# Optimization experiments

Hardware: AMD Instinct MI355X
Metric: run time of the kernel (lower is better)

The kernel has to match this reference:

```python
import jax, jax.numpy as jnp
import numpy as np

N_BR, D, SD, RH, MH, UD, NOBS, B = 4, 256, 64, 64, 128, 16, 25, 32768
LN_EPS = 1e-5

def setup_inputs() -> dict:
    key = jax.random.key(0)
    ks = jax.random.split(key, 16)
    meas_in = D + SD
    rnn_in = RH + UD
    return {
        "z_dyn": jax.random.normal(ks[0], (B, D), jnp.float32),
        "z_static": jax.random.normal(ks[1], (B, SD), jnp.float32),
        "dt": jnp.ones((1,), jnp.float32),
        "ut": jax.random.normal(ks[2], (B, UD), jnp.float32),
        "gates": jax.random.normal(ks[3], (N_BR, D), jnp.float32) * 0.1,
        "W1": jax.random.normal(ks[4], (N_BR, MH, meas_in), jnp.float32) * (1.0 / np.sqrt(meas_in)),
        "b1": jnp.zeros((N_BR, MH), jnp.float32),
        "gamma": jnp.ones((N_BR, MH), jnp.float32),
        "beta": jnp.zeros((N_BR, MH), jnp.float32),
        "W2": jax.random.normal(ks[5], (N_BR, RH, MH), jnp.float32) * (1.0 / np.sqrt(MH)),
        "b2": jnp.zeros((N_BR, RH), jnp.float32),
        "lam_real": jnp.zeros((N_BR, RH), jnp.float32),
        "lam_imag": jax.random.normal(ks[6], (N_BR, RH), jnp.float32) * 0.1,
        "Bmat": jax.random.normal(ks[7], (N_BR, RH, rnn_in), jnp.float32) * (1.0 / np.sqrt(rnn_in)),
        "Wout": jax.random.normal(ks[8], (N_BR, D, RH), jnp.float32) * (1.0 / np.sqrt(RH)),
        "C": jax.random.normal(ks[9], (NOBS, D), jnp.float32) * (1.0 / np.sqrt(D)),
        "D": jax.random.normal(ks[10], (NOBS, UD), jnp.float32) * (1.0 / np.sqrt(UD)),
    }

def reference(z_dyn, z_static, dt, ut, gates, W1, b1, gamma, beta, W2, b2,
              lam_real, lam_imag, Bmat, Wout, C, D):
    ut_dt = ut * dt  # [B,u]
    n, Bsz = gates.shape[0], z_dyn.shape[0]
    # spectral gate per branch: [n,B,d]
    zg = z_dyn[None] * jax.nn.sigmoid(gates)[:, None, :]
    zs = jnp.broadcast_to(z_static[None], (n, Bsz, z_static.shape[-1]))
    x = jnp.concatenate([zg, zs], axis=-1)  # [n,B,meas_in]
    # measurement MLP: Linear -> LayerNorm -> GELU -> Linear
    h = jnp.einsum('nbi,nhi->nbh', x, W1) + b1[:, None, :]
    mu = h.mean(-1, keepdims=True)
    var = ((h - mu) ** 2).mean(-1, keepdims=True)
    h = (h - mu) / jnp.sqrt(var + LN_EPS) * gamma[:, None, :] + beta[:, None, :]
    h = jax.nn.gelu(h, approximate=False)
    g = jnp.einsum('nbh,noh->nbo', h, W2) + b2[:, None, :]  # [n,B,rnn_h]
    u_b = jnp.broadcast_to(ut_dt[None], (n, Bsz, ut_dt.shape[-1]))
    inp = jnp.concatenate([g, u_b], axis=-1)  # [n,B,rnn_h+u]
    b_inp = jnp.einsum('nbi,nhi->nbh', inp, Bmat)
    # complex recurrence step from h0 = 0 (as in forward())
    mag = jax.nn.sigmoid(lam_real) * 0.99
    lam_r = mag * jnp.cos(lam_imag)
    lam_i = mag * jnp.sin(lam_imag)
    h0r = jnp.zeros_like(b_inp)
    h0i = jnp.zeros_like(b_inp)
    h_real = h0r * lam_r[:, None, :] - h0i * lam_i[:, None, :] + b_inp
    # output projection per branch, summed over branches
    z_next = jnp.einsum('nbh,ndh->bd', h_real, Wout)
    yt = z_next @ C.T + ut_dt @ D.T
    return (z_next, yt)
```

## Files before the change

### kernel.cpp

```cpp
#include <hip/hip_runtime.h>
#include <hip/hip_bf16.h>

#define B_ROWS 32768
#define LN_EPS 1e-5f

typedef __bf16 bf16;
using bf16x8 = __attribute__((ext_vector_type(8))) __bf16;
using f32x4  = __attribute__((ext_vector_type(4))) float;


__device__ __forceinline__ float gelu_exact(float x) {
  float s = x * 0.70710678118f;
  float a = fabsf(s);
  float t = __builtin_amdgcn_rcpf(fmaf(0.3275911f, a, 1.0f));
  float p = fmaf(fmaf(fmaf(fmaf(1.061405429f, t, -1.453152027f),
                           t, 1.421413741f), t, -0.284496736f), t, 0.254829592f) * t;
  float e = __expf(-s * s);
  float er = fmaf(-p, e, 1.0f);
  er = copysignf(er, s);
  return 0.5f * x * (1.0f + er);
}

__global__ __launch_bounds__(256) void prep_weights1(
    const float* __restrict__ gates, const float* __restrict__ W1,
    const float* __restrict__ Bmat,  const float* __restrict__ W2,
    const float* __restrict__ b2,    const float* __restrict__ Wout,
    const float* __restrict__ Cm,
    bf16* __restrict__ W1sw, float* __restrict__ Mtmp, float* __restrict__ cvec,
    float* __restrict__ CW)
{
  const int stride = gridDim.x * blockDim.x;
  const int id = blockIdx.x * blockDim.x + threadIdx.x;
  for (int o = id; o < 512 * 320; o += stride) {
    int e = o & 7, m = (o >> 3) & 15, q2 = (o >> 7) & 3, rest = o >> 9;
    int kk = rest % 10, G = rest / 10;
    int n = G * 16 + m, k = kk * 32 + q2 * 8 + e;
    float wv = W1[n * 320 + k];
    if (k < 256) {
      float g = gates[(n >> 7) * 256 + k];
      wv *= 1.f / (1.f + __expf(-g));
    }
    W1sw[o] = (bf16)wv;
  }
  for (int i = id; i < 4 * 64 * 128; i += stride) {
    int n = i >> 13, r = (i >> 7) & 63, h = i & 127;
    float s = 0.f;
    for (int j = 0; j < 64; ++j)
      s += Bmat[(n * 64 + r) * 80 + j] * W2[(n * 64 + j) * 128 + h];
    Mtmp[i] = s;
  }
  for (int i = id; i < 256; i += stride) {
    int n = i >> 6, r = i & 63;
    float s = 0.f;
    for (int j = 0; j < 64; ++j)
      s += Bmat[(n * 64 + r) * 80 + j] * b2[n * 64 + j];
    cvec[i] = s;
  }
  for (int i = id; i < 25 * 256; i += stride) {
    int o = i >> 8, nr = i & 255;
    float s = 0.f;
    for (int d = 0; d < 256; ++d)
      s += Cm[o * 256 + d] * Wout[((nr >> 6) * 256 + d) * 64 + (nr & 63)];
    CW[i] = s;
  }
}

__global__ __launch_bounds__(256) void prep_weights2(
    const float* __restrict__ Wout, const float* __restrict__ Bmat,
    const float* __restrict__ Mtmp, const float* __restrict__ cvec,
    const float* __restrict__ CW,   const float* __restrict__ Dm,
    bf16* __restrict__ Psw)
{
  const int stride = gridDim.x * blockDim.x;
  const int id = blockIdx.x * blockDim.x + threadIdx.x;
  for (int o = id; o < 320 * 544; o += stride) {
    int e = o & 7, m = (o >> 3) & 15, q2 = (o >> 7) & 3, rest = o >> 9;
    int kk2 = rest % 17, G2 = rest / 17;
    int dd = G2 * 16 + m, cc = kk2 * 32 + q2 * 8 + e;
    float s = 0.f;
    if (dd < 281) {
      const bool isC = (dd >= 256);
      const int oo = dd - 256;
      if (cc < 512) {
        int n = cc >> 7, h = cc & 127;
        for (int r = 0; r < 64; ++r) {
          float wv = isC ? CW[(oo * 4 + n) * 64 + r] : Wout[(n * 256 + dd) * 64 + r];
          s += wv * Mtmp[(n * 64 + r) * 128 + h];
        }
      } else if (cc < 528) {
        int u = cc - 512;
        for (int n = 0; n < 4; ++n)
          for (int r = 0; r < 64; ++r) {
            float wv = isC ? CW[(oo * 4 + n) * 64 + r] : Wout[(n * 256 + dd) * 64 + r];
            s += wv * Bmat[(n * 64 + r) * 80 + 64 + u];
          }
        if (isC) s += Dm[oo * 16 + u];
      } else if (cc == 528) {
        for (int n = 0; n < 4; ++n)
          for (int r = 0; r < 64; ++r) {
            float wv = isC ? CW[(oo * 4 + n) * 64 + r] : Wout[(n * 256 + dd) * 64 + r];
            s += wv * cvec[n * 64 + r];
          }
      }
    }
    Psw[o] = (bf16)s;
  }
}

__global__ __launch_bounds__(256, 2) void fused_main(
    const float* __restrict__ zdyn, const float* __restrict__ zst,
    const float* __restrict__ ut,   const float* __restrict__ dtp,
    const bf16* __restrict__ W1sw,  const bf16* __restrict__ Psw,
    const float* __restrict__ b1,   const float* __restrict__ gamma,
    const float* __restrict__ beta,
    float* __restrict__ Z, float* __restrict__ yt)
{
  __shared__ __align__(16) bf16 Xs[64 * 320];
  __shared__ __align__(16) bf16 Hc[64 * 128];
  __shared__ __align__(16) bf16 Ht[64 * 32];
  __shared__ float sgam[512], sbet[512], sb1[512];
  __shared__ float red[256], red2[256];
  __shared__ float smu[64], srs[64];

  const int t = threadIdx.x;
  const int lane = t & 63, m16 = lane & 15, q = lane >> 4;
  const int w = t >> 6;
  const int rowBase = blockIdx.x * 64;

  sgam[t] = gamma[t]; sbet[t] = beta[t]; sb1[t] = b1[t];
  sgam[t + 256] = gamma[t + 256]; sbet[t + 256] = beta[t + 256]; sb1[t + 256] = b1[t + 256];

  #pragma unroll
  for (int a = 0; a < 10; ++a) {
    int g = a * 256 + t;
    int row = g / 40, pos = g - row * 40;
    int kk = pos >> 2, pq = pos & 3;
    int lq = pq ^ ((row >> 1) & 3);
    int col = kk * 32 + lq * 8;
    const float* src = (col < 256) ? &zdyn[(size_t)(rowBase + row) * 256 + col]
                                   : &zst[(size_t)(rowBase + row) * 64 + (col - 256)];
    float4 v0 = *(const float4*)src;
    float4 v1 = *(const float4*)(src + 4);
    bf16x8 o;
    o[0]=(bf16)v0.x; o[1]=(bf16)v0.y; o[2]=(bf16)v0.z; o[3]=(bf16)v0.w;
    o[4]=(bf16)v1.x; o[5]=(bf16)v1.y; o[6]=(bf16)v1.z; o[7]=(bf16)v1.w;
    *(bf16x8*)&Xs[(size_t)((kk * 64 + row) * 4 + pq) * 8] = o;
  }
  {
    const float dtv = dtp[0];
    int r = t >> 2, pq = t & 3;
    int lq = pq ^ ((r >> 1) & 3);
    bf16x8 o;
    #pragma unroll
    for (int e = 0; e < 8; ++e) {
      int ci = lq * 8 + e;
      float v = (ci < 16) ? ut[(size_t)(rowBase + r) * 16 + ci] * dtv
                          : (ci == 16 ? 1.f : 0.f);
      o[e] = (bf16)v;
    }
    *(bf16x8*)&Ht[t * 8] = o;
  }
  __syncthreads();

  f32x4 accZ[4][5];
  #pragma unroll
  for (int i = 0; i < 4; ++i)
    #pragma unroll
    for (int j = 0; j < 5; ++j)
      #pragma unroll
      for (int r = 0; r < 4; ++r) accZ[i][j][r] = 0.f;

  #pragma unroll 1
  for (int c = 0; c < 4; ++c) {
    f32x4 acc1[4][2];
    #pragma unroll
    for (int i = 0; i < 4; ++i)
      #pragma unroll
      for (int j = 0; j < 2; ++j)
        #pragma unroll
        for (int r = 0; r < 4; ++r) acc1[i][j][r] = 0.f;

    #pragma unroll
    for (int kk = 0; kk < 10; ++kk) {
      bf16x8 bfr[2];
      #pragma unroll
      for (int j = 0; j < 2; ++j) {
        int G = c * 8 + w * 2 + j;
        bfr[j] = *(const bf16x8*)&W1sw[(size_t)(((G * 10 + kk) * 4 + q) * 16 + m16) * 8];
      }
      bf16x8 af[4];
      #pragma unroll
      for (int i = 0; i < 4; ++i) {
        int row = i * 16 + m16;
        af[i] = *(const bf16x8*)&Xs[(size_t)((kk * 64 + row) * 4 + (q ^ ((row >> 1) & 3))) * 8];
      }
      #pragma unroll
      for (int i = 0; i < 4; ++i)
        #pragma unroll
        for (int j = 0; j < 2; ++j)
          acc1[i][j] = __builtin_amdgcn_mfma_f32_16x16x32_bf16(af[i], bfr[j], acc1[i][j], 0, 0, 0);
    }

    __syncthreads();
    #pragma unroll
    for (int j = 0; j < 2; ++j) {
      int tc = w * 32 + j * 16 + m16;
      float bb = sb1[c * 128 + tc];
      int tk = tc >> 5, ci = tc & 31;
      int lq2 = ci >> 3, e2 = ci & 7;
      #pragma unroll
      for (int i = 0; i < 4; ++i)
        #pragma unroll
        for (int rr = 0; rr < 4; ++rr) {
          int row = i * 16 + q * 4 + rr;
          Hc[((tk * 64 + row) * 4 + (lq2 ^ ((row >> 1) & 3))) * 8 + e2] =
              (bf16)(acc1[i][j][rr] + bb);
        }
    }
    __syncthreads();
    {
      int row = t >> 2, tk = t & 3;
      float s = 0.f, s2 = 0.f;
      #pragma unroll
      for (int ch = 0; ch < 4; ++ch) {
        bf16x8 hv = *(const bf16x8*)&Hc[((tk * 64 + row) * 4 + ch) * 8];
        #pragma unroll
        for (int e = 0; e < 8; ++e) { float v = (float)hv[e]; s += v; s2 = fmaf(v, v, s2); }
      }
      red[t] = s; red2[t] = s2;
    }
    __syncthreads();
    if (t < 64) {
      float ss = red[t * 4] + red[t * 4 + 1] + red[t * 4 + 2] + red[t * 4 + 3];
      float qq = red2[t * 4] + red2[t * 4 + 1] + red2[t * 4 + 2] + red2[t * 4 + 3];
      float mu = ss * 0.0078125f;
      float var = qq * 0.0078125f - mu * mu;
      smu[t] = mu;
      srs[t] = rsqrtf(fmaxf(var, 0.f) + LN_EPS);
    }
    __syncthreads();
    #pragma unroll
    for (int a = 0; a < 4; ++a) {
      int id = a * 256 + t;
      int pq = id & 3, row = (id >> 2) & 63, tk = id >> 8;
      int lq = pq ^ ((row >> 1) & 3);
      int gcol = c * 128 + tk * 32 + lq * 8;
      bf16x8 hv = *(const bf16x8*)&Hc[id * 8];
      float mu = smu[row], rs = srs[row];
      bf16x8 ov;
      #pragma unroll
      for (int e = 0; e < 8; ++e) {
        float v = ((float)hv[e] - mu) * rs;
        v = fmaf(v, sgam[gcol + e], sbet[gcol + e]);
        ov[e] = (bf16)gelu_exact(v);
      }
      *(bf16x8*)&Hc[id * 8] = ov;
    }
    __syncthreads();

    #pragma unroll
    for (int tk = 0; tk < 4; ++tk) {
      int kk2 = c * 4 + tk;
      bf16x8 af[4], bfr[5];
      #pragma unroll
      for (int i = 0; i < 4; ++i) {
        int row = i * 16 + m16;
        af[i] = *(const bf16x8*)&Hc[((tk * 64 + row) * 4 + (q ^ ((row >> 1) & 3))) * 8];
      }
      #pragma unroll
      for (int j = 0; j < 5; ++j) {
        int G2 = w * 5 + j;
        bfr[j] = *(const bf16x8*)&Psw[(size_t)(((G2 * 17 + kk2) * 4 + q) * 16 + m16) * 8];
      }
      #pragma unroll
      for (int i = 0; i < 4; ++i)
        #pragma unroll
        for (int j = 0; j < 5; ++j)
          accZ[i][j] = __builtin_amdgcn_mfma_f32_16x16x32_bf16(af[i], bfr[j], accZ[i][j], 0, 0, 0);
    }
  }

  {
    bf16x8 af[4], bfr[5];
    #pragma unroll
    for (int i = 0; i < 4; ++i) {
      int row = i * 16 + m16;
      af[i] = *(const bf16x8*)&Ht[(row * 4 + (q ^ ((row >> 1) & 3))) * 8];
    }
    #pragma unroll
    for (int j = 0; j < 5; ++j) {
      int G2 = w * 5 + j;
      bfr[j] = *(const bf16x8*)&Psw[(size_t)(((G2 * 17 + 16) * 4 + q) * 16 + m16) * 8];
    }
    #pragma unroll
    for (int i = 0; i < 4; ++i)
      #pragma unroll
      for (int j = 0; j < 5; ++j)
        accZ[i][j] = __builtin_amdgcn_mfma_f32_16x16x32_bf16(af[i], bfr[j], accZ[i][j], 0, 0, 0);
  }

  #pragma unroll
  for (int i = 0; i < 4; ++i)
    #pragma unroll
    for (int j = 0; j < 5; ++j) {
      int col = w * 80 + j * 16 + m16;
      #pragma unroll
      for (int rr = 0; rr < 4; ++rr) {
        int row = rowBase + i * 16 + q * 4 + rr;
        if (col < 256) Z[(size_t)row * 256 + col] = accZ[i][j][rr];
        else if (col < 281) yt[(size_t)row * 25 + (col - 256)] = accZ[i][j][rr];
      }
    }
}

extern "C" void kernel_launch(void* const* d_in, const int* in_sizes, int n_in,
                              void* d_out, int out_size, void* d_ws, size_t ws_size,
                              hipStream_t stream) {
  const float* zdyn  = (const float*)d_in[0];
  const float* zst   = (const float*)d_in[1];
  const float* dtp   = (const float*)d_in[2];
  const float* ut    = (const float*)d_in[3];
  const float* gates = (const float*)d_in[4];
  const float* W1    = (const float*)d_in[5];
  const float* b1    = (const float*)d_in[6];
  const float* gamma = (const float*)d_in[7];
  const float* beta  = (const float*)d_in[8];
  const float* W2    = (const float*)d_in[9];
  const float* b2    = (const float*)d_in[10];
  const float* Bmat  = (const float*)d_in[13];
  const float* Wout  = (const float*)d_in[14];
  const float* Cm    = (const float*)d_in[15];
  const float* Dm    = (const float*)d_in[16];

  char* ws = (char*)d_ws;
  bf16*  W1sw = (bf16*)(ws);
  bf16*  Psw  = (bf16*)(ws + 327680);
  float* Mtmp = (float*)(ws + 675840);
  float* cvec = (float*)(ws + 806912);
  float* CW   = (float*)(ws + 807936);

  float* Z  = (float*)d_out;
  float* yt = Z + (size_t)B_ROWS * 256;

  hipLaunchKernelGGL(prep_weights1, dim3(128), dim3(256), 0, stream,
                     gates, W1, Bmat, W2, b2, Wout, Cm, W1sw, Mtmp, cvec, CW);
  hipLaunchKernelGGL(prep_weights2, dim3(256), dim3(256), 0, stream,
                     Wout, Bmat, Mtmp, cvec, CW, Dm, Psw);
  hipLaunchKernelGGL(fused_main, dim3(512), dim3(256), 0, stream,
                     zdyn, zst, ut, dtp, W1sw, Psw, b1, gamma, beta, Z, yt);
}
```

Before: 183.6 us.

## Compute LayerNorm stats in registers via shuffles and fuse GELU before LDS store

Adds the bias and computes LayerNorm partial sums directly from the MFMA accumulators, using lane shuffles and a small partial-sum array, instead of storing pre-LN values to LDS and reading them back. Normalization, affine and GELU are then applied in registers and written once to a re-laid-out Hc buffer. This removes one LDS round trip and a barrier per chunk. __syncthreads is also replaced with a raw lgkmcnt wait plus s_barrier. The risks are scattered scalar bf16 stores to LDS, which can cause bank conflicts, and more register pressure under the 2-waves launch bound.

After: 190.8 us. 3.9% more time.

```diff
diff --git a/kernel.cpp b/kernel.cpp
--- a/kernel.cpp
+++ b/kernel.cpp
@@ -8,6 +8,10 @@
 using bf16x8 = __attribute__((ext_vector_type(8))) __bf16;
 using f32x4  = __attribute__((ext_vector_type(4))) float;
 
+
+__device__ __forceinline__ void lds_barrier() {
+  asm volatile("s_waitcnt lgkmcnt(0)\n\ts_barrier" ::: "memory");
+}
 
 __device__ __forceinline__ float gelu_exact(float x) {
   float s = x * 0.70710678118f;
@@ -118,17 +122,18 @@
   __shared__ __align__(16) bf16 Xs[64 * 320];
   __shared__ __align__(16) bf16 Hc[64 * 128];
   __shared__ __align__(16) bf16 Ht[64 * 32];
-  __shared__ float sgam[512], sbet[512], sb1[512];
-  __shared__ float red[256], red2[256];
-  __shared__ float smu[64], srs[64];
+  __shared__ float sb1[512], sgam[512], sbet[512];
+  __shared__ float2 spart[64 * 17];
+  __shared__ __align__(16) float smu[64], srs[64];
 
   const int t = threadIdx.x;
   const int lane = t & 63, m16 = lane & 15, q = lane >> 4;
   const int w = t >> 6;
   const int rowBase = blockIdx.x * 64;
 
-  sgam[t] = gamma[t]; sbet[t] = beta[t]; sb1[t] = b1[t];
-  sgam[t + 256] = gamma[t + 256]; sbet[t + 256] = beta[t + 256]; sb1[t + 256] = b1[t + 256];
+  sb1[t] = b1[t];   sb1[t + 256] = b1[t + 256];
+  sgam[t] = gamma[t]; sgam[t + 256] = gamma[t + 256];
+  sbet[t] = beta[t];  sbet[t + 256] = beta[t + 256];
 
   #pragma unroll
   for (int a = 0; a < 10; ++a) {
@@ -160,7 +165,7 @@
     }
     *(bf16x8*)&Ht[t * 8] = o;
   }
-  __syncthreads();
+  lds_barrier();
 
   f32x4 accZ[4][5];
   #pragma unroll
@@ -201,71 +206,76 @@
           acc1[i][j] = __builtin_amdgcn_mfma_f32_16x16x32_bf16(af[i], bfr[j], acc1[i][j], 0, 0, 0);
     }
 
-    __syncthreads();
-    #pragma unroll
-    for (int j = 0; j < 2; ++j) {
-      int tc = w * 32 + j * 16 + m16;
-      float bb = sb1[c * 128 + tc];
-      int tk = tc >> 5, ci = tc & 31;
-      int lq2 = ci >> 3, e2 = ci & 7;
-      #pragma unroll
-      for (int i = 0; i < 4; ++i)
+    {
+      float b0v = sb1[c * 128 + w * 32 + m16];
+      float b1v = sb1[c * 128 + w * 32 + 16 + m16];
+      const int slot = w * 4 + (m16 >> 2);
+      #pragma unroll
+      for (int i = 0; i < 4; ++i) {
+        #pragma unroll
+        for (int rr = 0; rr < 4; ++rr) {
+          float v0 = acc1[i][0][rr] + b0v;
+          float v1 = acc1[i][1][rr] + b1v;
+          acc1[i][0][rr] = v0;
+          acc1[i][1][rr] = v1;
+          float s  = v0 + v1;
+          float s2 = fmaf(v0, v0, v1 * v1);
+          s  += __shfl_xor(s, 1);  s  += __shfl_xor(s, 2);
+          s2 += __shfl_xor(s2, 1); s2 += __shfl_xor(s2, 2);
+          if ((m16 & 3) == 0) {
+            int row = i * 16 + q * 4 + rr;
+            spart[row * 17 + slot] = make_float2(s, s2);
+          }
+        }
+      }
+    }
+    lds_barrier();
+    if (t < 64) {
+      float s = 0.f, s2 = 0.f;
+      #pragma unroll
+      for (int m = 0; m < 16; ++m) {
+        float2 p = spart[t * 17 + m];
+        s += p.x; s2 += p.y;
+      }
+      float mu = s * 0.0078125f;
+      float var = s2 * 0.0078125f - mu * mu;
+      smu[t] = mu;
+      srs[t] = rsqrtf(fmaxf(var, 0.f) + LN_EPS);
+    }
+    lds_barrier();
+
+    {
+      float g0 = sgam[c * 128 + w * 32 + m16];
+      float g1 = sgam[c * 128 + w * 32 + 16 + m16];
+      float be0 = sbet[c * 128 + w * 32 + m16];
+      float be1 = sbet[c * 128 + w * 32 + 16 + m16];
+      int col0 = w * 32 + m16, col1 = w * 32 + 16 + m16;
+      int cq0 = col0 >> 3, cq1 = col1 >> 3;
+      #pragma unroll
+      for (int i = 0; i < 4; ++i) {
+        f32x4 mu4 = *(const f32x4*)&smu[i * 16 + q * 4];
+        f32x4 rs4 = *(const f32x4*)&srs[i * 16 + q * 4];
         #pragma unroll
         for (int rr = 0; rr < 4; ++rr) {
           int row = i * 16 + q * 4 + rr;
-          Hc[((tk * 64 + row) * 4 + (lq2 ^ ((row >> 1) & 3))) * 8 + e2] =
-              (bf16)(acc1[i][j][rr] + bb);
+          int sw = (row >> 1) & 3;
+          float v0 = fmaf((acc1[i][0][rr] - mu4[rr]) * rs4[rr], g0, be0);
+          float v1 = fmaf((acc1[i][1][rr] - mu4[rr]) * rs4[rr], g1, be1);
+          Hc[row * 128 + (cq0 ^ sw) * 8 + (col0 & 7)] = (bf16)gelu_exact(v0);
+          Hc[row * 128 + (cq1 ^ sw) * 8 + (col1 & 7)] = (bf16)gelu_exact(v1);
         }
-    }
-    __syncthreads();
-    {
-      int row = t >> 2, tk = t & 3;
-      float s = 0.f, s2 = 0.f;
-      #pragma unroll
-      for (int ch = 0; ch < 4; ++ch) {
-        bf16x8 hv = *(const bf16x8*)&Hc[((tk * 64 + row) * 4 + ch) * 8];
-        #pragma unroll
-        for (int e = 0; e < 8; ++e) { float v = (float)hv[e]; s += v; s2 = fmaf(v, v, s2); }
-      }
-      red[t] = s; red2[t] = s2;
-    }
-    __syncthreads();
-    if (t < 64) {
-      float ss = red[t * 4] + red[t * 4 + 1] + red[t * 4 + 2] + red[t * 4 + 3];
-      float qq = red2[t * 4] + red2[t * 4 + 1] + red2[t * 4 + 2] + red2[t * 4 + 3];
-      float mu = ss * 0.0078125f;
-      float var = qq * 0.0078125f - mu * mu;
-      smu[t] = mu;
-      srs[t] = rsqrtf(fmaxf(var, 0.f) + LN_EPS);
-    }
-    __syncthreads();
-    #pragma unroll
-    for (int a = 0; a < 4; ++a) {
-      int id = a * 256 + t;
-      int pq = id & 3, row = (id >> 2) & 63, tk = id >> 8;
-      int lq = pq ^ ((row >> 1) & 3);
-      int gcol = c * 128 + tk * 32 + lq * 8;
-      bf16x8 hv = *(const bf16x8*)&Hc[id * 8];
-      float mu = smu[row], rs = srs[row];
-      bf16x8 ov;
-      #pragma unroll
-      for (int e = 0; e < 8; ++e) {
-        float v = ((float)hv[e] - mu) * rs;
-        v = fmaf(v, sgam[gcol + e], sbet[gcol + e]);
-        ov[e] = (bf16)gelu_exact(v);
-      }
-      *(bf16x8*)&Hc[id * 8] = ov;
-    }
-    __syncthreads();
-
-    #pragma unroll
-    for (int tk = 0; tk < 4; ++tk) {
-      int kk2 = c * 4 + tk;
+      }
+    }
+    lds_barrier();
+
+    #pragma unroll
+    for (int t2 = 0; t2 < 4; ++t2) {
+      int kk2 = c * 4 + t2;
       bf16x8 af[4], bfr[5];
       #pragma unroll
       for (int i = 0; i < 4; ++i) {
         int row = i * 16 + m16;
-        af[i] = *(const bf16x8*)&Hc[((tk * 64 + row) * 4 + (q ^ ((row >> 1) & 3))) * 8];
+        af[i] = *(const bf16x8*)&Hc[row * 128 + (((t2 * 4 + q) ^ ((row >> 1) & 3))) * 8];
       }
       #pragma unroll
       for (int j = 0; j < 5; ++j) {
@@ -303,11 +313,11 @@
   for (int i = 0; i < 4; ++i)
     #pragma unroll
     for (int j = 0; j < 5; ++j) {
-      int col = w * 80 + j * 16 + m16;
+      int col = (w * 5 + j) * 16 + m16;
       #pragma unroll
       for (int rr = 0; rr < 4; ++rr) {
         int row = rowBase + i * 16 + q * 4 + rr;
-        if (col < 256) Z[(size_t)row * 256 + col] = accZ[i][j][rr];
+        if (col < 256)      Z[(size_t)row * 256 + col] = accZ[i][j][rr];
         else if (col < 281) yt[(size_t)row * 25 + (col - 256)] = accZ[i][j][rr];
       }
     }
```

## Software-pipeline first GEMM of next chunk with second GEMM, lighter barriers

Applied to the files above, without the earlier changes.

Restructures the chunk loop so the first-layer MFMA for chunk c+1 is interleaved with the second-layer MFMA for chunk c, letting their independent work overlap within each wave. It also drops the separate LayerNorm statistics pass and its two barriers: each thread now recomputes mean and rstd from the partial sums. The remaining __syncthreads are replaced by a raw s_waitcnt lgkmcnt(0) + s_barrier. Keeping two accumulator sets live raises register pressure, which under launch_bounds(256,2) risks spills, and the inline-asm barrier skips waiting on global memory traffic.

Result: slower. 270.0 us (+47.1%).

```diff
diff --git a/kernel.cpp b/kernel.cpp
--- a/kernel.cpp
+++ b/kernel.cpp
@@ -8,6 +8,10 @@
 using bf16x8 = __attribute__((ext_vector_type(8))) __bf16;
 using f32x4  = __attribute__((ext_vector_type(4))) float;
 
+
+__device__ __forceinline__ void lds_barrier() {
+  asm volatile("s_waitcnt lgkmcnt(0)\n\ts_barrier" ::: "memory");
+}
 
 __device__ __forceinline__ float gelu_exact(float x) {
   float s = x * 0.70710678118f;
@@ -118,17 +122,17 @@
   __shared__ __align__(16) bf16 Xs[64 * 320];
   __shared__ __align__(16) bf16 Hc[64 * 128];
   __shared__ __align__(16) bf16 Ht[64 * 32];
-  __shared__ float sgam[512], sbet[512], sb1[512];
+  __shared__ float sb1[512], sgam[512], sbet[512];
   __shared__ float red[256], red2[256];
-  __shared__ float smu[64], srs[64];
 
   const int t = threadIdx.x;
   const int lane = t & 63, m16 = lane & 15, q = lane >> 4;
   const int w = t >> 6;
   const int rowBase = blockIdx.x * 64;
 
-  sgam[t] = gamma[t]; sbet[t] = beta[t]; sb1[t] = b1[t];
-  sgam[t + 256] = gamma[t + 256]; sbet[t + 256] = beta[t + 256]; sb1[t + 256] = b1[t + 256];
+  sb1[t] = b1[t];   sb1[t + 256] = b1[t + 256];
+  sgam[t] = gamma[t]; sgam[t + 256] = gamma[t + 256];
+  sbet[t] = beta[t];  sbet[t + 256] = beta[t + 256];
 
   #pragma unroll
   for (int a = 0; a < 10; ++a) {
@@ -160,7 +164,7 @@
     }
     *(bf16x8*)&Ht[t * 8] = o;
   }
-  __syncthreads();
+  lds_barrier();
 
   f32x4 accZ[4][5];
   #pragma unroll
@@ -170,38 +174,50 @@
       #pragma unroll
       for (int r = 0; r < 4; ++r) accZ[i][j][r] = 0.f;
 
-  #pragma unroll 1
-  for (int c = 0; c < 4; ++c) {
-    f32x4 acc1[4][2];
+  f32x4 acc1[4][2];
+
+  auto p1_step = [&](int cc, int kk) {
+    bf16x8 bfr0 = *(const bf16x8*)&W1sw[(size_t)((((cc * 8 + w * 2 + 0) * 10 + kk) * 4 + q) * 16 + m16) * 8];
+    bf16x8 bfr1 = *(const bf16x8*)&W1sw[(size_t)((((cc * 8 + w * 2 + 1) * 10 + kk) * 4 + q) * 16 + m16) * 8];
+    #pragma unroll
+    for (int i = 0; i < 4; ++i) {
+      int row = i * 16 + m16;
+      bf16x8 af = *(const bf16x8*)&Xs[(size_t)((kk * 64 + row) * 4 + (q ^ ((row >> 1) & 3))) * 8];
+      acc1[i][0] = __builtin_amdgcn_mfma_f32_16x16x32_bf16(af, bfr0, acc1[i][0], 0, 0, 0);
+      acc1[i][1] = __builtin_amdgcn_mfma_f32_16x16x32_bf16(af, bfr1, acc1[i][1], 0, 0, 0);
+    }
+  };
+  auto p2_step = [&](int cc, int t2) {
+    int kk2 = cc * 4 + t2;
+    bf16x8 bfr[5];
+    #pragma unroll
+    for (int j = 0; j < 5; ++j)
+      bfr[j] = *(const bf16x8*)&Psw[(size_t)((((w * 5 + j) * 17 + kk2) * 4 + q) * 16 + m16) * 8];
+    #pragma unroll
+    for (int i = 0; i < 4; ++i) {
+      int row = i * 16 + m16;
+      bf16x8 af = *(const bf16x8*)&Hc[((t2 * 64 + row) * 4 + (q ^ ((row >> 1) & 3))) * 8];
+      #pragma unroll
+      for (int j = 0; j < 5; ++j)
+        accZ[i][j] = __builtin_amdgcn_mfma_f32_16x16x32_bf16(af, bfr[j], accZ[i][j], 0, 0, 0);
+    }
+  };
+  auto p1_zero = [&]() {
     #pragma unroll
     for (int i = 0; i < 4; ++i)
       #pragma unroll
       for (int j = 0; j < 2; ++j)
         #pragma unroll
         for (int r = 0; r < 4; ++r) acc1[i][j][r] = 0.f;
-
-    #pragma unroll
-    for (int kk = 0; kk < 10; ++kk) {
-      bf16x8 bfr[2];
-      #pragma unroll
-      for (int j = 0; j < 2; ++j) {
-        int G = c * 8 + w * 2 + j;
-        bfr[j] = *(const bf16x8*)&W1sw[(size_t)(((G * 10 + kk) * 4 + q) * 16 + m16) * 8];
-      }
-      bf16x8 af[4];
-      #pragma unroll
-      for (int i = 0; i < 4; ++i) {
-        int row = i * 16 + m16;
-        af[i] = *(const bf16x8*)&Xs[(size_t)((kk * 64 + row) * 4 + (q ^ ((row >> 1) & 3))) * 8];
-      }
-      #pragma unroll
-      for (int i = 0; i < 4; ++i)
-        #pragma unroll
-        for (int j = 0; j < 2; ++j)
-          acc1[i][j] = __builtin_amdgcn_mfma_f32_16x16x32_bf16(af[i], bfr[j], acc1[i][j], 0, 0, 0);
-    }
-
-    __syncthreads();
+  };
+
+  p1_zero();
+  #pragma unroll
+  for (int kk = 0; kk < 10; ++kk) p1_step(0, kk);
+
+  #pragma unroll 1
+  for (int c = 0; c < 4; ++c) {
+    lds_barrier();
     #pragma unroll
     for (int j = 0; j < 2; ++j) {
       int tc = w * 32 + j * 16 + m16;
@@ -217,7 +233,7 @@
               (bf16)(acc1[i][j][rr] + bb);
         }
     }
-    __syncthreads();
+    lds_barrier();
     {
       int row = t >> 2, tk = t & 3;
       float s = 0.f, s2 = 0.f;
@@ -229,24 +245,19 @@
       }
       red[t] = s; red2[t] = s2;
     }
-    __syncthreads();
-    if (t < 64) {
-      float ss = red[t * 4] + red[t * 4 + 1] + red[t * 4 + 2] + red[t * 4 + 3];
-      float qq = red2[t * 4] + red2[t * 4 + 1] + red2[t * 4 + 2] + red2[t * 4 + 3];
-      float mu = ss * 0.0078125f;
-      float var = qq * 0.0078125f - mu * mu;
-      smu[t] = mu;
-      srs[t] = rsqrtf(fmaxf(var, 0.f) + LN_EPS);
-    }
-    __syncthreads();
+    lds_barrier();
     #pragma unroll
     for (int a = 0; a < 4; ++a) {
       int id = a * 256 + t;
       int pq = id & 3, row = (id >> 2) & 63, tk = id >> 8;
+      float ss = red[row * 4] + red[row * 4 + 1] + red[row * 4 + 2] + red[row * 4 + 3];
+      float qq = red2[row * 4] + red2[row * 4 + 1] + red2[row * 4 + 2] + red2[row * 4 + 3];
+      float mu = ss * 0.0078125f;
+      float var = qq * 0.0078125f - mu * mu;
+      float rs = rsqrtf(fmaxf(var, 0.f) + LN_EPS);
       int lq = pq ^ ((row >> 1) & 3);
       int gcol = c * 128 + tk * 32 + lq * 8;
       bf16x8 hv = *(const bf16x8*)&Hc[id * 8];
-      float mu = smu[row], rs = srs[row];
       bf16x8 ov;
       #pragma unroll
       for (int e = 0; e < 8; ++e) {
@@ -256,58 +267,41 @@
       }
       *(bf16x8*)&Hc[id * 8] = ov;
     }
-    __syncthreads();
-
-    #pragma unroll
-    for (int tk = 0; tk < 4; ++tk) {
-      int kk2 = c * 4 + tk;
-      bf16x8 af[4], bfr[5];
+    lds_barrier();
+
+    if (c < 3) {
+      p1_zero();
+      p2_step(c, 0); p1_step(c + 1, 0); p1_step(c + 1, 1);
+      p2_step(c, 1); p1_step(c + 1, 2); p1_step(c + 1, 3);
+      p2_step(c, 2); p1_step(c + 1, 4); p1_step(c + 1, 5);
+      p2_step(c, 3); p1_step(c + 1, 6); p1_step(c + 1, 7);
+      p1_step(c + 1, 8); p1_step(c + 1, 9);
+    } else {
+      p2_step(3, 0); p2_step(3, 1); p2_step(3, 2); p2_step(3, 3);
+      bf16x8 bfr[5];
+      #pragma unroll
+      for (int j = 0; j < 5; ++j)
+        bfr[j] = *(const bf16x8*)&Psw[(size_t)((((w * 5 + j) * 17 + 16) * 4 + q) * 16 + m16) * 8];
       #pragma unroll
       for (int i = 0; i < 4; ++i) {
         int row = i * 16 + m16;
-        af[i] = *(const bf16x8*)&Hc[((tk * 64 + row) * 4 + (q ^ ((row >> 1) & 3))) * 8];
-      }
-      #pragma unroll
-      for (int j = 0; j < 5; ++j) {
-        int G2 = w * 5 + j;
-        bfr[j] = *(const bf16x8*)&Psw[(size_t)(((G2 * 17 + kk2) * 4 + q) * 16 + m16) * 8];
-      }
-      #pragma unroll
-      for (int i = 0; i < 4; ++i)
+        bf16x8 af = *(const bf16x8*)&Ht[(row * 4 + (q ^ ((row >> 1) & 3))) * 8];
         #pragma unroll
         for (int j = 0; j < 5; ++j)
-          accZ[i][j] = __builtin_amdgcn_mfma_f32_16x16x32_bf16(af[i], bfr[j], accZ[i][j], 0, 0, 0);
-    }
-  }
-
-  {
-    bf16x8 af[4], bfr[5];
-    #pragma unroll
-    for (int i = 0; i < 4; ++i) {
-      int row = i * 16 + m16;
-      af[i] = *(const bf16x8*)&Ht[(row * 4 + (q ^ ((row >> 1) & 3))) * 8];
-    }
-    #pragma unroll
-    for (int j = 0; j < 5; ++j) {
-      int G2 = w * 5 + j;
-      bfr[j] = *(const bf16x8*)&Psw[(size_t)(((G2 * 17 + 16) * 4 + q) * 16 + m16) * 8];
-    }
-    #pragma unroll
-    for (int i = 0; i < 4; ++i)
-      #pragma unroll
-      for (int j = 0; j < 5; ++j)
-        accZ[i][j] = __builtin_amdgcn_mfma_f32_16x16x32_bf16(af[i], bfr[j], accZ[i][j], 0, 0, 0);
+          accZ[i][j] = __builtin_amdgcn_mfma_f32_16x16x32_bf16(af, bfr[j], accZ[i][j], 0, 0, 0);
+      }
+    }
   }
 
   #pragma unroll
   for (int i = 0; i < 4; ++i)
     #pragma unroll
     for (int j = 0; j < 5; ++j) {
-      int col = w * 80 + j * 16 + m16;
+      int col = (w * 5 + j) * 16 + m16;
       #pragma unroll
       for (int rr = 0; rr < 4; ++rr) {
         int row = rowBase + i * 16 + q * 4 + rr;
-        if (col < 256) Z[(size_t)row * 256 + col] = accZ[i][j][rr];
+        if (col < 256)      Z[(size_t)row * 256 + col] = accZ[i][j][rr];
         else if (col < 281) yt[(size_t)row * 25 + (col - 256)] = accZ[i][j][rr];
       }
     }
```
